# Kernel tuning notes

Measured on AMD Instinct MI355X. Metric: run time of the kernel, lower is better.

## Reference

```python
import jax, jax.numpy as jnp
import numpy as np

D, NH, E, F = 768, 12, 4, 3072            # embed dim, heads, experts/group, expert ffn (4*D)
NBLK, DEPTH = 2, 6                        # MoE blocks, DiT depth
N_A, N_B, N_C = 64, 32, 192               # group token counts
MA, FH, TC = 32, 8, 7                     # max_agents, future_horizon, traj_channels
BATCH = 8
T_TRAJ = MA * FH                          # 256 trajectory tokens
TFREQ = 256                               # sinusoidal timestep embedding dim
HD = D // NH

def _ln(x):
    mu = jnp.mean(x, -1, keepdims=True)
    v = jnp.var(x, -1, keepdims=True)
    return (x - mu) * jax.lax.rsqrt(v + 1e-6)

def _heads(x):
    b, n, _ = x.shape
    return x.reshape(b, n, NH, HD).transpose(0, 2, 1, 3)

def _attn(q, k, v):
    s = jnp.einsum('bhqd,bhkd->bhqk', q, k) * (HD ** -0.5)
    p = jax.nn.softmax(s, -1)
    o = jnp.einsum('bhqk,bhkd->bhqd', p, v)
    b, h, n, d = o.shape
    return o.transpose(0, 2, 1, 3).reshape(b, n, h * d)

def _cross(q_in, kv_in, W):
    # W: [4, D, D] = (Wq, Wk, Wv, Wo)
    q = _heads(q_in @ W[0]); k = _heads(kv_in @ W[1]); v = _heads(kv_in @ W[2])
    return _attn(q, k, v) @ W[3]

def _moe(x, Wr, W1, W2):
    # top-1 switch routing: gate = softmax prob of selected expert
    gates = jax.nn.softmax(x @ Wr)                       # [B,N,E]
    idx = jnp.argmax(gates, -1)                          # [B,N]
    gval = jnp.take_along_axis(gates, idx[..., None], -1)  # [B,N,1]
    h = jax.nn.gelu(jnp.einsum('bnd,edf->bnef', x, W1))
    y = jnp.einsum('bnef,efd->bned', h, W2)
    sel = jax.nn.one_hot(idx, W1.shape[0], dtype=x.dtype) * gval
    return jnp.einsum('bned,bne->bnd', y, sel)

def _forward(x_traj, tokens_A, tokens_B, tokens_C, W_traj, b_traj, W_ftime,
             Wt1, bt1, Wt2, bt2, moe_attn_W, moe_router, moe_W1, moe_W2,
             dit_qkv, dit_qkv_b, dit_proj, dit_proj_b, dit_mlp1, dit_mlp1_b,
             dit_mlp2, dit_mlp2_b, dit_ada, dit_ada_b,
             out_ada_W, out_ada_b, out_W, out_b, t):
    B = x_traj.shape[0]
    # timestep conditioning (DiT TimestepEmbedder)
    half = TFREQ // 2
    freqs = jnp.exp(-np.log(10000.0) * jnp.arange(half, dtype=jnp.float32) / half)
    ang = t.astype(jnp.float32)[:, None] * freqs
    temb = jnp.concatenate([jnp.cos(ang), jnp.sin(ang)], -1)     # [B,TFREQ]
    c = jax.nn.silu(temb @ Wt1 + bt1) @ Wt2 + bt2                # [B,D]

    # trajectory embedding + future-time embedding
    traj = x_traj.reshape(B, T_TRAJ, TC) @ W_traj + b_traj       # [B,256,D]
    traj = traj + jnp.tile(W_ftime, (MA, 1))[None]

    # StackedMoEBlocks: directed cross-attn A->C->B + per-group top-1 expert routing
    a, bg, cg = tokens_A, tokens_B, tokens_C
    for i in range(NBLK):
        cg = cg + _cross(_ln(cg), a, moe_attn_W[i, 0])
        bg = bg + _cross(_ln(bg), cg, moe_attn_W[i, 1])
        a = a + _moe(_ln(a), moe_router[i, 0], moe_W1[i, 0], moe_W2[i, 0])
        bg = bg + _moe(_ln(bg), moe_router[i, 1], moe_W1[i, 1], moe_W2[i, 1])
        cg = cg + _moe(_ln(cg), moe_router[i, 2], moe_W1[i, 2], moe_W2[i, 2])

    # DiT backbone over [traj | A | B | C], adaLN-zero conditioning on c
    x = jnp.concatenate([traj, a, bg, cg], 1)                    # [B,544,D]
    for i in range(DEPTH):
        mod = (jax.nn.silu(c) @ dit_ada[i] + dit_ada_b[i]).reshape(B, 6, 1, D)
        s1, sc1, g1, s2, sc2, g2 = [mod[:, j] for j in range(6)]
        h = _ln(x) * (1 + sc1) + s1
        qkv = h @ dit_qkv[i] + dit_qkv_b[i]
        q, k, v = jnp.split(qkv, 3, -1)
        x = x + g1 * (_attn(_heads(q), _heads(k), _heads(v)) @ dit_proj[i] + dit_proj_b[i])
        h = _ln(x) * (1 + sc2) + s2
        x = x + g2 * (jax.nn.gelu(h @ dit_mlp1[i] + dit_mlp1_b[i]) @ dit_mlp2[i] + dit_mlp2_b[i])

    # output head: final adaLN + projection to noise(+sigma), trajectory tokens only
    shift, scale = jnp.split(jax.nn.silu(c) @ out_ada_W + out_ada_b, 2, -1)
    h = _ln(x) * (1 + scale[:, None]) + shift[:, None]
    out = h @ out_W + out_b
    return out[:, :T_TRAJ].reshape(B, MA, FH, 2 * TC)

def setup_inputs() -> dict:
    key = jax.random.key(0)
    ks = jax.random.split(key, 24)
    n = jax.random.normal
    s = 0.02
    return dict(
        x_traj=n(ks[0], (BATCH, MA, FH, TC), jnp.float32),
        t=jax.random.randint(ks[1], (BATCH,), 0, 50),
        tokens_A=n(ks[2], (BATCH, N_A, D), jnp.float32),
        tokens_B=n(ks[3], (BATCH, N_B, D), jnp.float32),
        tokens_C=n(ks[4], (BATCH, N_C, D), jnp.float32),
        W_traj=n(ks[5], (TC, D)) * s, b_traj=jnp.zeros((D,)),
        W_ftime=n(ks[6], (FH, D)) * s,
        Wt1=n(ks[7], (TFREQ, D)) * s, bt1=jnp.zeros((D,)),
        Wt2=n(ks[8], (D, D)) * s, bt2=jnp.zeros((D,)),
        moe_attn_W=n(ks[9], (NBLK, 2, 4, D, D)) * s,
        moe_router=n(ks[10], (NBLK, 3, D, E)) * s,
        moe_W1=n(ks[11], (NBLK, 3, E, D, F)) * s,
        moe_W2=n(ks[12], (NBLK, 3, E, F, D)) * s,
        dit_qkv=n(ks[13], (DEPTH, D, 3 * D)) * s, dit_qkv_b=jnp.zeros((DEPTH, 3 * D)),
        dit_proj=n(ks[14], (DEPTH, D, D)) * s, dit_proj_b=jnp.zeros((DEPTH, D)),
        dit_mlp1=n(ks[15], (DEPTH, D, 4 * D)) * s, dit_mlp1_b=jnp.zeros((DEPTH, 4 * D)),
        dit_mlp2=n(ks[16], (DEPTH, 4 * D, D)) * s, dit_mlp2_b=jnp.zeros((DEPTH, D)),
        dit_ada=n(ks[17], (DEPTH, D, 6 * D)) * s, dit_ada_b=jnp.zeros((DEPTH, 6 * D)),
        out_ada_W=n(ks[18], (D, 2 * D)) * s, out_ada_b=jnp.zeros((2 * D,)),
        out_W=n(ks[19], (D, 2 * TC)) * s, out_b=jnp.zeros((2 * TC,)),
    )

def reference(x_traj, t, tokens_A, tokens_B, tokens_C, W_traj, b_traj, W_ftime,
              Wt1, bt1, Wt2, bt2, moe_attn_W, moe_router, moe_W1, moe_W2,
              dit_qkv, dit_qkv_b, dit_proj, dit_proj_b, dit_mlp1, dit_mlp1_b,
              dit_mlp2, dit_mlp2_b, dit_ada, dit_ada_b,
              out_ada_W, out_ada_b, out_W, out_b):
    return _forward(x_traj, tokens_A, tokens_B, tokens_C, W_traj, b_traj, W_ftime,
                    Wt1, bt1, Wt2, bt2, moe_attn_W, moe_router, moe_W1, moe_W2,
                    dit_qkv, dit_qkv_b, dit_proj, dit_proj_b, dit_mlp1, dit_mlp1_b,
                    dit_mlp2, dit_mlp2_b, dit_ada, dit_ada_b,
                    out_ada_W, out_ada_b, out_W, out_b, t)
```

## Files before the change

### kernel.cpp

```cpp
#include <hip/hip_runtime.h>
#include <hip/hip_bf16.h>
#include <math.h>

#define D 768
#define NH 12
#define HD 64
#define NEXP 4
#define FF 3072
#define NBLK 2
#define DEPTH 6
#define NA 64
#define NB 32
#define NC 192
#define BATCH 8
#define TTRAJ 256
#define NTOK 544
#define MAXTOK 1536
#define MOER 2304

typedef __attribute__((ext_vector_type(8))) short short8v;
typedef __attribute__((ext_vector_type(4))) float f32x4;

__device__ __forceinline__ float siluf(float v) { return v / (1.f + expf(-v)); }
__device__ __forceinline__ float geluf(float v) {
// ... 76 lines not shown
        __syncthreads();
        #pragma unroll
        for (int kk = 0; kk < 16; ++kk) {
            float a[4], bv[4];
            #pragma unroll
            for (int i = 0; i < 4; ++i) a[i] = As[kk][ty * 4 + i];
            #pragma unroll
            for (int j = 0; j < 4; ++j) bv[j] = Bs[kk][tx * 4 + j];
            #pragma unroll
            for (int i = 0; i < 4; ++i)
                #pragma unroll
                for (int j = 0; j < 4; ++j) acc[i][j] += a[i] * bv[j];
        }
        __syncthreads();
    }
    #pragma unroll
    for (int i = 0; i < 4; ++i) {
        int gr = row0 + ty * 4 + i; if (gr >= M) continue;
        #pragma unroll
        for (int j = 0; j < 4; ++j) {
            int gc = col0 + tx * 4 + j; if (gc >= N) continue;
            float v = acc[i][j] + (bias ? bias[gc] : 0.f);
            if (ACT == 1) v = siluf(v);
            if (ACT == 2) v = geluf(v);
            C[(size_t)gr * ldc + gc] = v;
        }
    }
}

__global__ __launch_bounds__(256) void transpose_cvt(
    const float* __restrict__ in, unsigned short* __restrict__ out, int K, int N)
{
    __shared__ unsigned short Ls[64][72];
    const float* src = in + (size_t)blockIdx.z * K * N;
    unsigned short* dst = out + (size_t)blockIdx.z * K * N;
    int k0 = blockIdx.y * 64, n0 = blockIdx.x * 64;
    int tid = threadIdx.x;
    int r = tid >> 2, c0 = (tid & 3) * 16;
    {
        const float* sp = src + (size_t)(k0 + r) * N + n0 + c0;
        #pragma unroll
        for (int j = 0; j < 16; j += 4) {
            float4 f = *(const float4*)(sp + j);
            Ls[c0 + j + 0][r] = f2bf(f.x);
            Ls[c0 + j + 1][r] = f2bf(f.y);
            Ls[c0 + j + 2][r] = f2bf(f.z);
            Ls[c0 + j + 3][r] = f2bf(f.w);
        }
    }
    __syncthreads();
    {
        unsigned short tmp[16];
        #pragma unroll
        for (int j = 0; j < 16; ++j) tmp[j] = Ls[r][c0 + j];
        unsigned short* dp = dst + (size_t)(n0 + r) * K + k0 + c0;
        *(short8v*)dp = *(short8v*)tmp;
        *(short8v*)(dp + 8) = *(short8v*)(tmp + 8);
    }
}

template<int ACT, int OUT, int TN>
__global__ __launch_bounds__(256) void gemm_lds(
    const unsigned short* __restrict__ A,
    const unsigned short* __restrict__ BT,
    const float* __restrict__ bias,
    float* __restrict__ Cf, unsigned short* __restrict__ Cb, int ldc,
    int K, int qscale_cols,
    const float* __restrict__ mod, int modstride, int gchunk, int ntok, int mrows,
    size_t bt_zs = 0, size_t bias_zs = 0, size_t c_zs = 0)
{
    constexpr int NCF = TN / 32;
    constexpr int NBS = TN / 64;
    if (bt_zs) BT += (size_t)blockIdx.z * bt_zs;
    if (bias && bias_zs) bias += (size_t)blockIdx.z * bias_zs;
    if (c_zs) { if (Cf) Cf += (size_t)blockIdx.z * c_zs; if (Cb) Cb += (size_t)blockIdx.z * c_zs; }
    __shared__ unsigned short As[2][128 * 32];
    __shared__ unsigned short Bs[2][TN * 32];
    int tid = threadIdx.x, w = tid >> 6, lane = tid & 63;
    int row0 = blockIdx.y * 128, col0 = blockIdx.x * TN;
    int wrow = (w >> 1) * 64, wcol = (w & 1) * (TN / 2);
    int lr = lane & 15, g = lane >> 4;
    f32x4 acc[4][NCF] = {};

    int ra[2], ka[2], la[2];
    #pragma unroll
    for (int i = 0; i < 2; ++i) {
        int off = tid * 16 + i * 4096;
        int row = off >> 6;
        int slot = (off >> 4) & 3;
        ra[i] = row;
        ka[i] = (slot ^ ((row >> 1) & 3)) * 8;
        la[i] = off >> 1;
    }
    int nt = K >> 5, cur = 0;
    #pragma unroll
    for (int i = 0; i < 2; ++i)
        gl16(A + (size_t)(row0 + ra[i]) * K + ka[i], &As[0][la[i]]);
    #pragma unroll
    for (int i = 0; i < NBS; ++i)
        gl16(BT + (size_t)(col0 + ra[i]) * K + ka[i], &Bs[0][la[i]]);

    for (int t = 0; t < nt; ++t) {
        __syncthreads();
        if (t + 1 < nt) {
            int k0 = (t + 1) << 5;
            #pragma unroll
            for (int i = 0; i < 2; ++i)
                gl16(A + (size_t)(row0 + ra[i]) * K + k0 + ka[i], &As[cur ^ 1][la[i]]);
            #pragma unroll
            for (int i = 0; i < NBS; ++i)
                gl16(BT + (size_t)(col0 + ra[i]) * K + k0 + ka[i], &Bs[cur ^ 1][la[i]]);
        }
        short8v av[4], bv[NCF];
        #pragma unroll
        for (int mr = 0; mr < 4; ++mr) {
            int row = wrow + mr * 16 + lr;
            av[mr] = *(const short8v*)&As[cur][row * 32 + (g ^ ((row >> 1) & 3)) * 8];
        }
        #pragma unroll
        for (int nc = 0; nc < NCF; ++nc) {
            int row = wcol + nc * 16 + lr;
            bv[nc] = *(const short8v*)&Bs[cur][row * 32 + (g ^ ((row >> 1) & 3)) * 8];
        }
        #pragma unroll
        for (int mr = 0; mr < 4; ++mr)
            #pragma unroll
            for (int nc = 0; nc < NCF; ++nc)
                acc[mr][nc] = __builtin_amdgcn_mfma_f32_16x16x32_bf16(
                    av[mr], bv[nc], acc[mr][nc], 0, 0, 0);
        cur ^= 1;
    }
    int rbase = g * 4;
    #pragma unroll
    for (int mr = 0; mr < 4; ++mr) {
        #pragma unroll
        for (int nc = 0; nc < NCF; ++nc) {
            int gc = col0 + wcol + nc * 16 + lr;
            float bb = bias ? bias[gc] : 0.f;
            #pragma unroll
            for (int r = 0; r < 4; ++r) {
                int gr = row0 + wrow + mr * 16 + rbase + r;
                if (gr >= mrows) continue;
                float v = acc[mr][nc][r] + bb;
                if (ACT == 1) v = siluf(v);
                if (ACT == 2) v = geluf(v);
                if (OUT == 0) {
                    Cf[(size_t)gr * ldc + gc] = v;
                } else if (OUT == 1) {
                    if (gc < qscale_cols) v *= 0.125f;
                    Cb[(size_t)gr * ldc + gc] = f2bf(v);
                } else {
                    float gg = 1.f;
                    if (mod) gg = mod[(size_t)(gr / ntok) * modstride + gchunk * D + gc];
                    Cf[(size_t)gr * ldc + gc] += gg * v;
                }
            }
        }
    }
}

template<int ACT>
__global__ __launch_bounds__(512, 4) void gemm_lds256(
    const unsigned short* __restrict__ A,
    const unsigned short* __restrict__ BT,
    const float* __restrict__ bias,
    unsigned short* __restrict__ Cb, int ldc,
    int K, int qscale_cols)
{
    __shared__ unsigned short As[2][256 * 32];
    __shared__ unsigned short Bs[2][128 * 32];
    int tid = threadIdx.x, w = tid >> 6, lane = tid & 63;
    int row0 = blockIdx.y * 256, col0 = blockIdx.x * 128;
    int wrow = (w >> 1) * 64, wcol = (w & 1) * 64;
    int lr = lane & 15, g = lane >> 4;
    f32x4 acc[4][4] = {};

    int ra[2], ka[2], la[2];
    #pragma unroll
    for (int i = 0; i < 2; ++i) {
        int off = tid * 16 + i * 8192;
        int row = off >> 6;
        int slot = (off >> 4) & 3;
        ra[i] = row;
        ka[i] = (slot ^ ((row >> 1) & 3)) * 8;
        la[i] = off >> 1;
    }
    int rb, kb, lb;
    {
        int off = tid * 16;
        int row = off >> 6;
        int slot = (off >> 4) & 3;
        rb = row;
        kb = (slot ^ ((row >> 1) & 3)) * 8;
        lb = off >> 1;
    }
    int nt = K >> 5, cur = 0;
    #pragma unroll
    for (int i = 0; i < 2; ++i)
        gl16(A + (size_t)(row0 + ra[i]) * K + ka[i], &As[0][la[i]]);
    gl16(BT + (size_t)(col0 + rb) * K + kb, &Bs[0][lb]);

    for (int t = 0; t < nt; ++t) {
        __syncthreads();
        if (t + 1 < nt) {
            int k0 = (t + 1) << 5;
            #pragma unroll
            for (int i = 0; i < 2; ++i)
                gl16(A + (size_t)(row0 + ra[i]) * K + k0 + ka[i], &As[cur ^ 1][la[i]]);
            gl16(BT + (size_t)(col0 + rb) * K + k0 + kb, &Bs[cur ^ 1][lb]);
        }
        short8v av[4], bv[4];
        #pragma unroll
        for (int mr = 0; mr < 4; ++mr) {
            int row = wrow + mr * 16 + lr;
            av[mr] = *(const short8v*)&As[cur][row * 32 + (g ^ ((row >> 1) & 3)) * 8];
        }
        #pragma unroll
        for (int nc = 0; nc < 4; ++nc) {
            int row = wcol + nc * 16 + lr;
            bv[nc] = *(const short8v*)&Bs[cur][row * 32 + (g ^ ((row >> 1) & 3)) * 8];
        }
        #pragma unroll
        for (int mr = 0; mr < 4; ++mr)
            #pragma unroll
            for (int nc = 0; nc < 4; ++nc)
                acc[mr][nc] = __builtin_amdgcn_mfma_f32_16x16x32_bf16(
                    av[mr], bv[nc], acc[mr][nc], 0, 0, 0);
        cur ^= 1;
    }
    int rbase = g * 4;
    int wrow2 = (w >> 1) * 64;
    (void)wrow2;
    #pragma unroll
    for (int mr = 0; mr < 4; ++mr) {
        #pragma unroll
        for (int nc = 0; nc < 4; ++nc) {
            int gc = col0 + wcol + nc * 16 + lr;
            float bb = bias ? bias[gc] : 0.f;
            #pragma unroll
            for (int r = 0; r < 4; ++r) {
                int gr = row0 + wrow + mr * 16 + rbase + r;
                float v = acc[mr][nc][r] + bb;
                if (ACT == 2) v = geluf(v);
                if (gc < qscale_cols) v *= 0.125f;
                Cb[(size_t)gr * ldc + gc] = f2bf(v);
            }
        }
    }
}

template<int PHASE>
__global__ __launch_bounds__(256) void moe_lds(
    const unsigned short* __restrict__ A,
    const unsigned short* __restrict__ BTconv,
    float* __restrict__ Cf, unsigned short* __restrict__ Cb,
    const int* __restrict__ cnt, const int* __restrict__ list,
    const float* __restrict__ gval, int RT, int egbase)
{
    constexpr int K  = (PHASE == 1) ? 768 : 3072;
    constexpr int TN = (PHASE == 1) ? 128 : 64;
    constexpr int NCF = TN / 32;
    constexpr int NBS = TN / 64;
    int egl = blockIdx.y / RT, rt = blockIdx.y % RT;
    int eg = egbase + egl;
    int c0 = cnt[eg];
    int mbase = rt * 128;
    if (mbase >= c0) return;
    int mcount = min(128, c0 - mbase);
    __shared__ int toks[128];
    int tid = threadIdx.x, w = tid >> 6, lane = tid & 63;
    if (tid < 128) toks[tid] = list[eg * MAXTOK + mbase + min(tid, mcount - 1)];
    __syncthreads();

    __shared__ unsigned short As[2][128 * 32];
    __shared__ unsigned short Bs[2][TN * 32];
    const unsigned short* BT = BTconv + (size_t)egl * (768 * 3072);
    int col0 = blockIdx.x * TN;
    int wrow = (w >> 1) * 64, wcol = (w & 1) * (TN / 2);
    int lr = lane & 15, g = lane >> 4;
    f32x4 acc[4][NCF] = {};

    int ra[2], ka[2], la[2], tok_s[2];
    #pragma unroll
    for (int i = 0; i < 2; ++i) {
        int off = tid * 16 + i * 4096;
        int row = off >> 6;
        int slot = (off >> 4) & 3;
        ra[i] = row;
        ka[i] = (slot ^ ((row >> 1) & 3)) * 8;
        la[i] = off >> 1;
        tok_s[i] = toks[row];
    }
    int nt = K >> 5, cur = 0;
    #pragma unroll
    for (int i = 0; i < 2; ++i)
        gl16(A + (size_t)tok_s[i] * K + ka[i], &As[0][la[i]]);
    #pragma unroll
    for (int i = 0; i < NBS; ++i)
        gl16(BT + (size_t)(col0 + ra[i]) * K + ka[i], &Bs[0][la[i]]);

    for (int t = 0; t < nt; ++t) {
        __syncthreads();
        if (t + 1 < nt) {
            int k0 = (t + 1) << 5;
            #pragma unroll
            for (int i = 0; i < 2; ++i)
                gl16(A + (size_t)tok_s[i] * K + k0 + ka[i], &As[cur ^ 1][la[i]]);
            #pragma unroll
            for (int i = 0; i < NBS; ++i)
                gl16(BT + (size_t)(col0 + ra[i]) * K + k0 + ka[i], &Bs[cur ^ 1][la[i]]);
        }
        short8v av[4], bv[NCF];
        #pragma unroll
        for (int mr = 0; mr < 4; ++mr) {
            int row = wrow + mr * 16 + lr;
            av[mr] = *(const short8v*)&As[cur][row * 32 + (g ^ ((row >> 1) & 3)) * 8];
        }
        #pragma unroll
        for (int nc = 0; nc < NCF; ++nc) {
            int row = wcol + nc * 16 + lr;
            bv[nc] = *(const short8v*)&Bs[cur][row * 32 + (g ^ ((row >> 1) & 3)) * 8];
        }
        #pragma unroll
        for (int mr = 0; mr < 4; ++mr)
            #pragma unroll
            for (int nc = 0; nc < NCF; ++nc)
                acc[mr][nc] = __builtin_amdgcn_mfma_f32_16x16x32_bf16(
                    av[mr], bv[nc], acc[mr][nc], 0, 0, 0);
        cur ^= 1;
    }
    int rbase = g * 4;
    #pragma unroll
    for (int mr = 0; mr < 4; ++mr) {
        #pragma unroll
        for (int r = 0; r < 4; ++r) {
            int m = wrow + mr * 16 + rbase + r;
            if (m >= mcount) continue;
            int tok = toks[m];
            #pragma unroll
            for (int nc = 0; nc < NCF; ++nc) {
                int gc = col0 + wcol + nc * 16 + lr;
                float v = acc[mr][nc][r];
                if (PHASE == 1) Cb[(size_t)tok * 3072 + gc] = f2bf(geluf(v));
                else            Cf[(size_t)tok * 768 + gc] += gval[tok] * v;
            }
        }
    }
}

__global__ __launch_bounds__(256) void ln_kernel(
    const float* __restrict__ X, unsigned short* __restrict__ Y, int R, int ntok,
    const float* __restrict__ mod, int modstride, int shift_chunk, int scale_chunk)
{
    int r = blockIdx.x;
    if (r >= R) return;
    const float* xr = X + (size_t)r * D;
    int tid = threadIdx.x;
    int lane = tid & 63, wid = tid >> 6;
    float v0 = xr[tid], v1 = xr[tid + 256], v2 = xr[tid + 512];
    float s = v0 + v1 + v2;
    float s2 = v0 * v0 + v1 * v1 + v2 * v2;
    for (int off = 32; off > 0; off >>= 1) {
        s += __shfl_xor(s, off, 64);
        s2 += __shfl_xor(s2, off, 64);
    }
    __shared__ float shs[4], shs2[4];
    if (lane == 0) { shs[wid] = s; shs2[wid] = s2; }
    __syncthreads();
    float tot = shs[0] + shs[1] + shs[2] + shs[3];
    float tot2 = shs2[0] + shs2[1] + shs2[2] + shs2[3];
    float mu = tot * (1.f / 768.f);
    float var = tot2 * (1.f / 768.f) - mu * mu;
    float rs = rsqrtf(var + 1e-6f);
    int bb = r / ntok;
    float vv[3] = {v0, v1, v2};
    #pragma unroll
    for (int j = 0; j < 3; ++j) {
        int col = tid + j * 256;
        float nrm = (vv[j] - mu) * rs;
        float y = nrm;
        if (mod) {
            float scv = mod[(size_t)bb * modstride + scale_chunk * D + col];
            float shv = mod[(size_t)bb * modstride + shift_chunk * D + col];
            y = nrm * (1.f + scv) + shv;
        }
        Y[(size_t)r * D + col] = f2bf(y);
    }
}

__global__ __launch_bounds__(512) void attn_mfma(
    const unsigned short* __restrict__ Qp, int ldq, int qoff,
    const unsigned short* __restrict__ Kp, int ldk, int koff,
    const unsigned short* __restrict__ Vp, int ldv, int voff,
    unsigned short* __restrict__ O, int ldo,
    int Nq, int Nkv)
{
    __shared__ unsigned short Qs[128 * 64];
    __shared__ unsigned short Ks[64 * 64];
    __shared__ unsigned short Vs[64 * 64];
    __shared__ unsigned short Ps[128 * 64];
    int h = blockIdx.y, b = blockIdx.z, q0 = blockIdx.x * 128;
    int tid = threadIdx.x, w = tid >> 6, lane = tid & 63;
    int wrow = w * 16;
    int lr = lane & 15, g = lane >> 4;

    {
        int srow = tid >> 2, sc = (tid & 3) * 16;
        int gr = min(q0 + srow, Nq - 1);
        const unsigned short* qp = Qp + (size_t)(b * Nq + gr) * ldq + qoff + h * 64 + sc;
        short8v v0 = *(const short8v*)qp, v1 = *(const short8v*)(qp + 8);
        int s0 = sc >> 3;
        *(short8v*)&Qs[srow * 64 + (s0 ^ (srow & 7)) * 8] = v0;
        *(short8v*)&Qs[srow * 64 + ((s0 + 1) ^ (srow & 7)) * 8] = v1;
    }
    float m_r[4] = {-1e30f, -1e30f, -1e30f, -1e30f};
    float l_r[4] = {};
    f32x4 acc0 = {}, acc1 = {}, acc2 = {}, acc3 = {};

    for (int kv0 = 0; kv0 < Nkv; kv0 += 64) {
        {
            int t2 = tid & 255;
            int srow = t2 >> 2, sc = (t2 & 3) * 16;
            int gc = min(kv0 + srow, Nkv - 1);
            if (tid < 256) {
                const unsigned short* kp = Kp + (size_t)(b * Nkv + gc) * ldk + koff + h * 64 + sc;
                short8v v0 = *(const short8v*)kp, v1 = *(const short8v*)(kp + 8);
                int s0 = sc >> 3;
                *(short8v*)&Ks[srow * 64 + (s0 ^ (srow & 7)) * 8] = v0;
                *(short8v*)&Ks[srow * 64 + ((s0 + 1) ^ (srow & 7)) * 8] = v1;
            } else {
                const unsigned short* vp = Vp + (size_t)(b * Nkv + gc) * ldv + voff + h * 64 + sc;
                #pragma unroll
                for (int j = 0; j < 16; ++j) {
                    int d = sc + j;
                    Vs[d * 64 + (((srow >> 3) ^ (d & 7)) * 8) + (srow & 7)] = vp[j];
                }
            }
        }
        __syncthreads();
        short8v aq0, aq1;
        {
            int row = wrow + lr;
            aq0 = *(const short8v*)&Qs[row * 64 + ((0 + g) ^ (row & 7)) * 8];
            aq1 = *(const short8v*)&Qs[row * 64 + ((4 + g) ^ (row & 7)) * 8];
        }
        f32x4 sf[4];
        #pragma unroll
        for (int nc = 0; nc < 4; ++nc) {
            int row = nc * 16 + lr;
            short8v bk0 = *(const short8v*)&Ks[row * 64 + ((0 + g) ^ (row & 7)) * 8];
            short8v bk1 = *(const short8v*)&Ks[row * 64 + ((4 + g) ^ (row & 7)) * 8];
            f32x4 z = {};
            z = __builtin_amdgcn_mfma_f32_16x16x32_bf16(aq0, bk0, z, 0, 0, 0);
            sf[nc] = __builtin_amdgcn_mfma_f32_16x16x32_bf16(aq1, bk1, z, 0, 0, 0);
        }
        bool val0 = (kv0 + 0 * 16 + lr) < Nkv;
        bool val1 = (kv0 + 1 * 16 + lr) < Nkv;
        bool val2 = (kv0 + 2 * 16 + lr) < Nkv;
        bool val3 = (kv0 + 3 * 16 + lr) < Nkv;
        float fs[4];
        #pragma unroll
        for (int r = 0; r < 4; ++r) {
            float s0 = val0 ? sf[0][r] : -1e30f;
            float s1 = val1 ? sf[1][r] : -1e30f;
            float s2 = val2 ? sf[2][r] : -1e30f;
            float s3 = val3 ? sf[3][r] : -1e30f;
            float mx = fmaxf(fmaxf(s0, s1), fmaxf(s2, s3));
            mx = fmaxf(mx, __shfl_xor(mx, 1, 64));
            mx = fmaxf(mx, __shfl_xor(mx, 2, 64));
            mx = fmaxf(mx, __shfl_xor(mx, 4, 64));
            mx = fmaxf(mx, __shfl_xor(mx, 8, 64));
            float mn = fmaxf(m_r[r], mx);
            fs[r] = __expf(m_r[r] - mn);
            m_r[r] = mn;
            float p0 = __expf(s0 - mn), p1 = __expf(s1 - mn);
            float p2 = __expf(s2 - mn), p3 = __expf(s3 - mn);
            float rsum = p0 + p1 + p2 + p3;
            rsum += __shfl_xor(rsum, 1, 64);
            rsum += __shfl_xor(rsum, 2, 64);
            rsum += __shfl_xor(rsum, 4, 64);
            rsum += __shfl_xor(rsum, 8, 64);
            l_r[r] = l_r[r] * fs[r] + rsum;
            int ql = wrow + g * 4 + r;
            int base = ql * 64;
            int x7 = ql & 7;
            Ps[base + (((0 * 16 + lr) >> 3) ^ x7) * 8 + (lr & 7)] = f2bf(p0);
            Ps[base + (((1 * 16 + lr) >> 3) ^ x7) * 8 + (lr & 7)] = f2bf(p1);
            Ps[base + (((2 * 16 + lr) >> 3) ^ x7) * 8 + (lr & 7)] = f2bf(p2);
            Ps[base + (((3 * 16 + lr) >> 3) ^ x7) * 8 + (lr & 7)] = f2bf(p3);
            acc0[r] *= fs[r]; acc1[r] *= fs[r]; acc2[r] *= fs[r]; acc3[r] *= fs[r];
        }
        __syncthreads();
        short8v ap0, ap1;
        {
            int row = wrow + lr;
            ap0 = *(const short8v*)&Ps[row * 64 + ((0 + g) ^ (row & 7)) * 8];
            ap1 = *(const short8v*)&Ps[row * 64 + ((4 + g) ^ (row & 7)) * 8];
        }
        {
            int row = 0 * 16 + lr;
            short8v b0 = *(const short8v*)&Vs[row * 64 + ((0 + g) ^ (row & 7)) * 8];
            short8v b1 = *(const short8v*)&Vs[row * 64 + ((4 + g) ^ (row & 7)) * 8];
            acc0 = __builtin_amdgcn_mfma_f32_16x16x32_bf16(ap0, b0, acc0, 0, 0, 0);
            acc0 = __builtin_amdgcn_mfma_f32_16x16x32_bf16(ap1, b1, acc0, 0, 0, 0);
        }
        {
            int row = 1 * 16 + lr;
            short8v b0 = *(const short8v*)&Vs[row * 64 + ((0 + g) ^ (row & 7)) * 8];
            short8v b1 = *(const short8v*)&Vs[row * 64 + ((4 + g) ^ (row & 7)) * 8];
            acc1 = __builtin_amdgcn_mfma_f32_16x16x32_bf16(ap0, b0, acc1, 0, 0, 0);
            acc1 = __builtin_amdgcn_mfma_f32_16x16x32_bf16(ap1, b1, acc1, 0, 0, 0);
        }
        {
            int row = 2 * 16 + lr;
            short8v b0 = *(const short8v*)&Vs[row * 64 + ((0 + g) ^ (row & 7)) * 8];
            short8v b1 = *(const short8v*)&Vs[row * 64 + ((4 + g) ^ (row & 7)) * 8];
            acc2 = __builtin_amdgcn_mfma_f32_16x16x32_bf16(ap0, b0, acc2, 0, 0, 0);
            acc2 = __builtin_amdgcn_mfma_f32_16x16x32_bf16(ap1, b1, acc2, 0, 0, 0);
        }
        {
            int row = 3 * 16 + lr;
            short8v b0 = *(const short8v*)&Vs[row * 64 + ((0 + g) ^ (row & 7)) * 8];
            short8v b1 = *(const short8v*)&Vs[row * 64 + ((4 + g) ^ (row & 7)) * 8];
            acc3 = __builtin_amdgcn_mfma_f32_16x16x32_bf16(ap0, b0, acc3, 0, 0, 0);
            acc3 = __builtin_amdgcn_mfma_f32_16x16x32_bf16(ap1, b1, acc3, 0, 0, 0);
        }
        __syncthreads();
    }
    #pragma unroll
    for (int r = 0; r < 4; ++r) {
        int ql = wrow + g * 4 + r;
        if (q0 + ql >= Nq) continue;
        float rl = 1.f / l_r[r];
        unsigned short* op = O + (size_t)(b * Nq + q0 + ql) * ldo + h * 64 + lr;
        op[0]  = f2bf(acc0[r] * rl);
        op[16] = f2bf(acc1[r] * rl);
        op[32] = f2bf(acc2[r] * rl);
        op[48] = f2bf(acc3[r] * rl);
    }
}

__global__ __launch_bounds__(64) void router_kernel(
    const unsigned short* __restrict__ X, const float* __restrict__ WrBase,
    int* __restrict__ idx, float* __restrict__ gval)
{
    int tkn = blockIdx.x; int lane = threadIdx.x;
    int grp = (tkn >= 768) ? 2 : (tkn >= 512 ? 1 : 0);
    const float* Wr = WrBase + (size_t)grp * D * NEXP;
    const unsigned short* xr = X + (size_t)tkn * D;
    float p0 = 0, p1 = 0, p2 = 0, p3 = 0;
    for (int dd = lane; dd < D; dd += 64) {
        float xv = bf2f(xr[dd]);
        const float* wq = Wr + dd * 4;
        p0 += xv * wq[0]; p1 += xv * wq[1]; p2 += xv * wq[2]; p3 += xv * wq[3];
    }
    for (int off = 32; off > 0; off >>= 1) {
        p0 += __shfl_xor(p0, off, 64); p1 += __shfl_xor(p1, off, 64);
        p2 += __shfl_xor(p2, off, 64); p3 += __shfl_xor(p3, off, 64);
    }
    if (lane == 0) {
        float best = p0; int e = 0;
        if (p1 > best) { best = p1; e = 1; }
        if (p2 > best) { best = p2; e = 2; }
        if (p3 > best) { best = p3; e = 3; }
        float sum = expf(p0 - best) + expf(p1 - best) + expf(p2 - best) + expf(p3 - best);
        idx[tkn] = grp * 4 + e;
        gval[tkn] = 1.f / sum;
    }
}

__global__ __launch_bounds__(256) void scatter_kernel(
    const int* __restrict__ idx, int* __restrict__ cnt,
    int* __restrict__ list, int ntok)
{
    __shared__ int lcnt[12];
    int tid = threadIdx.x;
    if (tid < 12) lcnt[tid] = 0;
    __syncthreads();
    for (int i = tid; i < ntok; i += 256) {
        int e = idx[i];
        int pos = atomicAdd(&lcnt[e], 1);
        list[e * MAXTOK + pos] = i;
    }
    __syncthreads();
    if (tid < 12) cnt[tid] = lcnt[tid];
}

__global__ void concat_kernel(const float* __restrict__ traj, const float* __restrict__ a,
                              const float* __restrict__ bg, const float* __restrict__ cg,
                              float* __restrict__ x, int total)
{
    int i = blockIdx.x * blockDim.x + threadIdx.x;
    if (i >= total) return;
    int col = i % D;
    int r = i / D;
    int n = r % NTOK, b = r / NTOK;
    float v;
    if (n < 256)      v = traj[((size_t)b * 256 + n) * D + col];
    else if (n < 320) v = a[((size_t)b * 64 + (n - 256)) * D + col];
    else if (n < 352) v = bg[((size_t)b * 32 + (n - 320)) * D + col];
    else              v = cg[((size_t)b * 192 + (n - 352)) * D + col];
    x[i] = v;
}

__global__ void head_prep(const float* __restrict__ W, unsigned short* __restrict__ WT14) {
    int i = blockIdx.x * blockDim.x + threadIdx.x;
    if (i >= 14 * 768) return;
    int o = i / 768, d = i % 768;
    WT14[i] = f2bf(W[d * 14 + o]);
}

__global__ __launch_bounds__(64) void head_kernel(
    const unsigned short* __restrict__ lnb, const unsigned short* __restrict__ WT14,
    const float* __restrict__ bias, float* __restrict__ out)
{
    int r = blockIdx.x;
    int b = r >> 8, n = r & 255;
    const unsigned short* hrow = lnb + (size_t)(b * NTOK + n) * D;
    int l = threadIdx.x;
    if (l >= 56) return;
    int o = l >> 2, p = l & 3;
    const unsigned short* hp = hrow + p * 192;
    const unsigned short* wp = WT14 + o * 768 + p * 192;
    float acc = 0.f;
    for (int i = 0; i < 192; i += 8) {
        short8v hv = *(const short8v*)(hp + i);
        short8v wv = *(const short8v*)(wp + i);
        #pragma unroll
        for (int j = 0; j < 8; ++j)
            acc += bf2f((unsigned short)hv[j]) * bf2f((unsigned short)wv[j]);
    }
    acc += __shfl_xor(acc, 1, 64);
    acc += __shfl_xor(acc, 2, 64);
    if (p == 0) out[(size_t)r * 14 + o] = acc + bias[o];
}

static inline void tcvt(const float* W, unsigned short* WT, int K, int N, int z, hipStream_t s) {
    transpose_cvt<<<dim3(N / 64, K / 64, z), 256, 0, s>>>(W, WT, K, N);
}
static inline void g_bf(int act, const unsigned short* A, const unsigned short* BT,
                        const float* bias, unsigned short* C, int ldc,
                        int M, int N, int K, int qcols, hipStream_t s)
{
    if (M % 256 == 0 && N % 128 == 0 && N >= 2304) {
        dim3 g(N / 128, M / 256);
        if (act == 2) gemm_lds256<2><<<g, 512, 0, s>>>(A, BT, bias, C, ldc, K, qcols);
        else          gemm_lds256<0><<<g, 512, 0, s>>>(A, BT, bias, C, ldc, K, qcols);
        return;
    }
    if (N != 768) {
        dim3 g(N / 128, M / 128);
        if (act == 2) gemm_lds<2, 1, 128><<<g, 256, 0, s>>>(A, BT, bias, nullptr, C, ldc, K, qcols, nullptr, 0, 0, 1, 1 << 30);
        else          gemm_lds<0, 1, 128><<<g, 256, 0, s>>>(A, BT, bias, nullptr, C, ldc, K, qcols, nullptr, 0, 0, 1, 1 << 30);
    } else {
        dim3 g(N / 64, M / 128);
        if (act == 2) gemm_lds<2, 1, 64><<<g, 256, 0, s>>>(A, BT, bias, nullptr, C, ldc, K, qcols, nullptr, 0, 0, 1, 1 << 30);
        else          gemm_lds<0, 1, 64><<<g, 256, 0, s>>>(A, BT, bias, nullptr, C, ldc, K, qcols, nullptr, 0, 0, 1, 1 << 30);
    }
}
static inline void g_res(const unsigned short* A, const unsigned short* BT,
                         const float* bias, float* C, int ldc, int M, int N, int K,
                         const float* mod, int modstride, int gchunk, int ntok, hipStream_t s)
{
    dim3 g(N / 64, M / 128);
    gemm_lds<0, 2, 64><<<g, 256, 0, s>>>(A, BT, bias, C, nullptr, ldc, K, 0, mod, modstride, gchunk, ntok, 1 << 30);
}

extern "C" void kernel_launch(void* const* d_in, const int* in_sizes, int n_in,
                              void* d_out, int out_size, void* d_ws, size_t ws_size,
                              hipStream_t stream)
{
    const float* x_traj   = (const float*)d_in[0];
    const int*   t_arr    = (const int*)d_in[1];
    const float* tokA     = (const float*)d_in[2];
    const float* tokB     = (const float*)d_in[3];
    const float* tokC     = (const float*)d_in[4];
    const float* W_traj   = (const float*)d_in[5];
    const float* b_traj   = (const float*)d_in[6];
    const float* W_ftime  = (const float*)d_in[7];
    const float* Wt1      = (const float*)d_in[8];
    const float* bt1      = (const float*)d_in[9];
    const float* Wt2      = (const float*)d_in[10];
    const float* bt2      = (const float*)d_in[11];
    const float* moe_attn = (const float*)d_in[12];
    const float* moe_rout = (const float*)d_in[13];
    const float* moe_W1   = (const float*)d_in[14];
    const float* moe_W2   = (const float*)d_in[15];
    const float* dit_qkv  = (const float*)d_in[16];
    const float* dit_qkvb = (const float*)d_in[17];
    const float* dit_proj = (const float*)d_in[18];
    const float* dit_projb= (const float*)d_in[19];
    const float* dit_mlp1 = (const float*)d_in[20];
    const float* dit_mlp1b= (const float*)d_in[21];
    const float* dit_mlp2 = (const float*)d_in[22];
    const float* dit_mlp2b= (const float*)d_in[23];
    const float* dit_ada  = (const float*)d_in[24];
    const float* dit_adab = (const float*)d_in[25];
    const float* out_adaW = (const float*)d_in[26];
    const float* out_adab = (const float*)d_in[27];
    const float* out_W    = (const float*)d_in[28];
    const float* out_b    = (const float*)d_in[29];
    float* out = (float*)d_out;
    float* ws = (float*)d_ws;

    const size_t o_cnt  = 14336;
    const size_t o_idx  = 14400;
    const size_t o_gval = 16704;
    const size_t o_list = 19008;
    const size_t o_traj = 66624;
    const size_t o_a    = 1639488;
    const size_t o_bg   = 2032704;
    const size_t o_cg   = 2229312;
    const size_t o_x    = 3408960;
    const size_t o_lnb  = 6751296;
    const size_t o_qkvb = 8422464;
    const size_t o_attnO= 13435968;
    const size_t o_h    = 15107136;
    const size_t o_kvbf = 23561280;
    const size_t o_wt   = 24151104;
    const size_t o_wt14 = 28869696;
    const size_t o_tembP= 28875072;
    const size_t o_ub   = 28891456;
    const size_t o_scb  = 28940608;
    const size_t o_mod  = o_traj;
    const size_t o_mod2 = o_traj + 221184;

    const size_t o_wqkv  = 29000000;
    const size_t o_wproj = 34308416;
    const size_t o_wmlp1 = 36077888;
    const size_t o_wmlp2 = 43155776;
    const size_t o_wada  = 50233664;
    const size_t o_wada2 = 60850496;
    const size_t o_wcross= 61440320;
    const size_t o_wmoe1 = 66158912;
    const size_t o_wmoe2 = 94470464;
    const bool bigw = ws_size >= (size_t)123000000 * 4;

    int* cnt_p  = (int*)(ws + o_cnt);
    int* idx_p  = (int*)(ws + o_idx);
    int* list_p = (int*)(ws + o_list);
    float* gval_p = ws + o_gval;
    unsigned short* lnb  = (unsigned short*)(ws + o_lnb);
    unsigned short* qkvb = (unsigned short*)(ws + o_qkvb);
    unsigned short* attO = (unsigned short*)(ws + o_attnO);
    unsigned short* hbuf = (unsigned short*)(ws + o_h);
    unsigned short* kvbf = (unsigned short*)(ws + o_kvbf);
    unsigned short* wt   = (unsigned short*)(ws + o_wt);
    unsigned short* wt14 = (unsigned short*)(ws + o_wt14);
    unsigned short* tembP= (unsigned short*)(ws + o_tembP);
    unsigned short* ub   = (unsigned short*)(ws + o_ub);
    unsigned short* scb  = (unsigned short*)(ws + o_scb);
    unsigned short* wqkvS = (unsigned short*)(ws + o_wqkv);
    unsigned short* wprojS= (unsigned short*)(ws + o_wproj);
    unsigned short* wmlp1S= (unsigned short*)(ws + o_wmlp1);
    unsigned short* wmlp2S= (unsigned short*)(ws + o_wmlp2);
    unsigned short* wadaS = (unsigned short*)(ws + o_wada);
    unsigned short* wada2S= (unsigned short*)(ws + o_wada2);
    unsigned short* wcrossS=(unsigned short*)(ws + o_wcross);
    unsigned short* wmoe1S= (unsigned short*)(ws + o_wmoe1);
    unsigned short* wmoe2S= (unsigned short*)(ws + o_wmoe2);
    unsigned short* c_q  = qkvb;
    unsigned short* c_kv = qkvb + 1179648;

    const size_t WSZ = (size_t)D * D;

    gemm_act<0><<<dim3(12, 32), 256, 0, stream>>>(x_traj, 7, W_traj, D, b_traj,
                                                  ws + o_traj, D, BATCH * TTRAJ, D, 7);
    add_ftime<<<(BATCH * TTRAJ * D + 255) / 256, 256, 0, stream>>>(ws + o_traj, W_ftime, BATCH * TTRAJ * D);

    hipError_t e1 = hipMemcpyAsync(ws + o_a, tokA, (size_t)BATCH * NA * D * 4, hipMemcpyDeviceToDevice, stream); (void)e1;
    hipError_t e2 = hipMemcpyAsync(ws + o_bg, tokB, (size_t)BATCH * NB * D * 4, hipMemcpyDeviceToDevice, stream); (void)e2;
    hipError_t e3 = hipMemcpyAsync(ws + o_cg, tokC, (size_t)BATCH * NC * D * 4, hipMemcpyDeviceToDevice, stream); (void)e3;
    head_prep<<<42, 256, 0, stream>>>(out_W, wt14);

    if (bigw) {
        tcvt(dit_qkv,  wqkvS,  D, 3 * D, DEPTH, stream);
        tcvt(dit_proj, wprojS, D, D, DEPTH, stream);
        tcvt(dit_mlp1, wmlp1S, D, FF, DEPTH, stream);
        tcvt(dit_mlp2, wmlp2S, FF, D, DEPTH, stream);
        tcvt(dit_ada,  wadaS,  D, 6 * D, DEPTH, stream);
        tcvt(out_adaW, wada2S, D, 2 * D, 1, stream);
        tcvt(moe_attn, wcrossS, D, D, NBLK * 2 * 4, stream);
        tcvt(moe_W1,   wmoe1S, D, FF, NBLK * 3 * NEXP, stream);
        tcvt(moe_W2,   wmoe2S, FF, D, NBLK * 3 * NEXP, stream);
    }

    timestep_kernel<<<128, 256, 0, stream>>>(t_arr, tembP);
    tcvt(Wt1, wt, 256, D, 1, stream);
    gemm_lds<1, 1, 64><<<dim3(12, 1), 256, 0, stream>>>(
        tembP, wt, bt1, nullptr, ub, D, 256, 0, nullptr, 0, 0, 1, 128);
    tcvt(Wt2, wt, D, D, 1, stream);
    gemm_lds<1, 1, 64><<<dim3(12, 1), 256, 0, stream>>>(
        ub, wt, bt2, nullptr, scb, D, D, 0, nullptr, 0, 0, 1, 128);

    for (int i = 0; i < NBLK; ++i) {
        {
            const unsigned short* Wc;
            if (bigw) Wc = wcrossS + (size_t)(i * 2 + 0) * 4 * WSZ;
            else { tcvt(moe_attn + (size_t)(i * 2 + 0) * 4 * WSZ, wt, D, D, 4, stream); Wc = wt; }
            ln_kernel<<<BATCH * NC, 256, 0, stream>>>(ws + o_cg, lnb, BATCH * NC, 1, nullptr, 0, 0, 0);
            g_bf(0, lnb, Wc, nullptr, c_q, D, BATCH * NC, D, D, 768, stream);
            cvt_bf16<<<(BATCH * NA * D / 8 + 255) / 256, 256, 0, stream>>>(ws + o_a, kvbf, BATCH * NA * D / 8);
            g_bf(0, kvbf, Wc + 1 * WSZ, nullptr, c_kv, 2 * D, BATCH * NA, 2 * D, D, 0, stream);
            attn_mfma<<<dim3((NC + 127) / 128, NH, BATCH), 512, 0, stream>>>(
                c_q, D, 0, c_kv, 2 * D, 0, c_kv, 2 * D, D, attO, D, NC, NA);
            g_res(attO, Wc + 3 * WSZ, nullptr, ws + o_cg, D, BATCH * NC, D, D, nullptr, 0, 0, 1, stream);
        }
        {
            const unsigned short* Wc;
            if (bigw) Wc = wcrossS + (size_t)(i * 2 + 1) * 4 * WSZ;
            else { tcvt(moe_attn + (size_t)(i * 2 + 1) * 4 * WSZ, wt, D, D, 4, stream); Wc = wt; }
            ln_kernel<<<BATCH * NB, 256, 0, stream>>>(ws + o_bg, lnb, BATCH * NB, 1, nullptr, 0, 0, 0);
            g_bf(0, lnb, Wc, nullptr, c_q, D, BATCH * NB, D, D, 768, stream);
            cvt_bf16<<<(BATCH * NC * D / 8 + 255) / 256, 256, 0, stream>>>(ws + o_cg, kvbf, BATCH * NC * D / 8);
            g_bf(0, kvbf, Wc + 1 * WSZ, nullptr, c_kv, 2 * D, BATCH * NC, 2 * D, D, 0, stream);
            attn_mfma<<<dim3(1, NH, BATCH), 512, 0, stream>>>(
                c_q, D, 0, c_kv, 2 * D, 0, c_kv, 2 * D, D, attO, D, NB, NC);
            g_res(attO, Wc + 3 * WSZ, nullptr, ws + o_bg, D, BATCH * NB, D, D, nullptr, 0, 0, 1, stream);
        }
        ln_kernel<<<MOER, 256, 0, stream>>>(ws + o_a, lnb, MOER, 1, nullptr, 0, 0, 0);
        router_kernel<<<MOER, 64, 0, stream>>>(lnb, moe_rout + (size_t)(i * 3) * D * NEXP, idx_p, gval_p);
        scatter_kernel<<<1, 256, 0, stream>>>(idx_p, cnt_p, list_p, MOER);
        const int RT = 12;
        if (bigw) {
            moe_lds<1><<<dim3(24, 12 * RT), 256, 0, stream>>>(
                lnb, wmoe1S + (size_t)(i * 3) * NEXP * D * FF, nullptr, hbuf,
                cnt_p, list_p, gval_p, RT, 0);
            moe_lds<2><<<dim3(12, 12 * RT), 256, 0, stream>>>(
                hbuf, wmoe2S + (size_t)(i * 3) * NEXP * D * FF, ws + o_a, nullptr,
                cnt_p, list_p, gval_p, RT, 0);
        } else {
            for (int g = 0; g < 3; ++g) {
                tcvt(moe_W1 + (size_t)(i * 3 + g) * NEXP * D * FF, wt, D, FF, NEXP, stream);
                moe_lds<1><<<dim3(24, 4 * RT), 256, 0, stream>>>(
                    lnb, wt, nullptr, hbuf, cnt_p, list_p, gval_p, RT, g * 4);
                tcvt(moe_W2 + (size_t)(i * 3 + g) * NEXP * FF * D, wt, FF, D, NEXP, stream);
                moe_lds<2><<<dim3(12, 4 * RT), 256, 0, stream>>>(
                    hbuf, wt, ws + o_a, nullptr, cnt_p, list_p, gval_p, RT, g * 4);
            }
        }
    }

    concat_kernel<<<(BATCH * NTOK * D + 255) / 256, 256, 0, stream>>>(
        ws + o_traj, ws + o_a, ws + o_bg, ws + o_cg, ws + o_x, BATCH * NTOK * D);

    if (bigw) {
        gemm_lds<0, 0, 128><<<dim3(36, 1, DEPTH), 256, 0, stream>>>(
            scb, wadaS, dit_adab, ws + o_mod, nullptr, 6 * D, D, 0,
            nullptr, 0, 0, 1, 8,
            (size_t)D * 6 * D, (size_t)6 * D, (size_t)8 * 6 * D);
        gemm_lds<0, 0, 128><<<dim3(12, 1), 256, 0, stream>>>(
            scb, wada2S, out_adab, ws + o_mod2, nullptr, 2 * D, D, 0, nullptr, 0, 0, 1, 8);
    } else {
        for (int i = 0; i < DEPTH; ++i) {
            tcvt(dit_ada + (size_t)i * D * 6 * D, wt, D, 6 * D, 1, stream);
            gemm_lds<0, 0, 128><<<dim3(36, 1), 256, 0, stream>>>(
                scb, wt, dit_adab + (size_t)i * 6 * D, ws + o_mod + (size_t)i * 8 * 6 * D,
                nullptr, 6 * D, D, 0, nullptr, 0, 0, 1, 8);
        }
        tcvt(out_adaW, wt, D, 2 * D, 1, stream);
        gemm_lds<0, 0, 128><<<dim3(12, 1), 256, 0, stream>>>(
            scb, wt, out_adab, ws + o_mod2, nullptr, 2 * D, D, 0, nullptr, 0, 0, 1, 8);
    }

    const int R = BATCH * NTOK;
    for (int i = 0; i < DEPTH; ++i) {
        const float* mod_l = ws + o_mod + (size_t)i * 8 * 6 * D;
        const unsigned short *Wq = nullptr, *Wp = nullptr, *Wm1 = nullptr, *Wm2 = nullptr;
        if (bigw) {
            Wq  = wqkvS  + (size_t)i * D * 3 * D;
            Wp  = wprojS + (size_t)i * D * D;
            Wm1 = wmlp1S + (size_t)i * D * FF;
            Wm2 = wmlp2S + (size_t)i * D * FF;
        }
        ln_kernel<<<R, 256, 0, stream>>>(ws + o_x, lnb, R, NTOK, mod_l, 6 * D, 0, 1);
        if (!bigw) { tcvt(dit_qkv + (size_t)i * D * 3 * D, wt, D, 3 * D, 1, stream); Wq = wt; }
        g_bf(0, lnb, Wq, dit_qkvb + (size_t)i * 3 * D, qkvb, 3 * D, R, 3 * D, D, 768, stream);
        attn_mfma<<<dim3((NTOK + 127) / 128, NH, BATCH), 512, 0, stream>>>(
            qkvb, 3 * D, 0, qkvb, 3 * D, D, qkvb, 3 * D, 2 * D, attO, D, NTOK, NTOK);
        if (!bigw) { tcvt(dit_proj + (size_t)i * D * D, wt, D, D, 1, stream); Wp = wt; }
        g_res(attO, Wp, dit_projb + (size_t)i * D, ws + o_x, D, R, D, D,
              mod_l, 6 * D, 2, NTOK, stream);
        ln_kernel<<<R, 256, 0, stream>>>(ws + o_x, lnb, R, NTOK, mod_l, 6 * D, 3, 4);
        if (!bigw) { tcvt(dit_mlp1 + (size_t)i * D * FF, wt, D, FF, 1, stream); Wm1 = wt; }
        g_bf(2, lnb, Wm1, dit_mlp1b + (size_t)i * FF, hbuf, FF, R, FF, D, 0, stream);
        if (!bigw) { tcvt(dit_mlp2 + (size_t)i * FF * D, wt, FF, D, 1, stream); Wm2 = wt; }
        g_res(hbuf, Wm2, dit_mlp2b + (size_t)i * D, ws + o_x, D, R, D, FF,
              mod_l, 6 * D, 5, NTOK, stream);
    }

    ln_kernel<<<R, 256, 0, stream>>>(ws + o_x, lnb, R, NTOK, ws + o_mod2, 2 * D, 0, 1);
    head_kernel<<<BATCH * TTRAJ, 64, 0, stream>>>(lnb, wt14, out_b, out);
}
```

Before: 2.379 ms.

## Store residual streams in bf16 instead of fp32 throughout the pipeline

Switches the residual buffers for the token groups and the DiT hidden state from fp32 to bf16. Residual GEMM epilogues now read-modify-write bf16, LayerNorm reads bf16, and the input token copies become direct bf16 conversions, which drops the separate cvt_bf16 passes before the K/V projections. This halves residual memory traffic and removes some kernels, but residual accumulation in bf16 loses precision across 6 DiT layers and the MoE blocks, which may hurt accuracy.

```diff
diff --git a/kernel.cpp b/kernel.cpp
--- a/kernel.cpp
+++ b/kernel.cpp
@@ -252,7 +252,8 @@
                 } else {
                     float gg = 1.f;
                     if (mod) gg = mod[(size_t)(gr / ntok) * modstride + gchunk * D + gc];
-                    Cf[(size_t)gr * ldc + gc] += gg * v;
+                    size_t idx = (size_t)gr * ldc + gc;
+                    Cb[idx] = f2bf(bf2f(Cb[idx]) + gg * v);
                 }
             }
         }
@@ -329,8 +330,6 @@
         cur ^= 1;
     }
     int rbase = g * 4;
-    int wrow2 = (w >> 1) * 64;
-    (void)wrow2;
     #pragma unroll
     for (int mr = 0; mr < 4; ++mr) {
         #pragma unroll
@@ -353,7 +352,7 @@
 __global__ __launch_bounds__(256) void moe_lds(
     const unsigned short* __restrict__ A,
     const unsigned short* __restrict__ BTconv,
-    float* __restrict__ Cf, unsigned short* __restrict__ Cb,
+    unsigned short* __restrict__ Cb,
     const int* __restrict__ cnt, const int* __restrict__ list,
     const float* __restrict__ gval, int RT, int egbase)
 {
@@ -442,22 +441,25 @@
                 int gc = col0 + wcol + nc * 16 + lr;
                 float v = acc[mr][nc][r];
                 if (PHASE == 1) Cb[(size_t)tok * 3072 + gc] = f2bf(geluf(v));
-                else            Cf[(size_t)tok * 768 + gc] += gval[tok] * v;
+                else {
+                    size_t idx = (size_t)tok * 768 + gc;
+                    Cb[idx] = f2bf(bf2f(Cb[idx]) + gval[tok] * v);
+                }
             }
         }
     }
 }
 
 __global__ __launch_bounds__(256) void ln_kernel(
-    const float* __restrict__ X, unsigned short* __restrict__ Y, int R, int ntok,
+    const unsigned short* __restrict__ X, unsigned short* __restrict__ Y, int R, int ntok,
     const float* __restrict__ mod, int modstride, int shift_chunk, int scale_chunk)
 {
     int r = blockIdx.x;
     if (r >= R) return;
-    const float* xr = X + (size_t)r * D;
+    const unsigned short* xr = X + (size_t)r * D;
     int tid = threadIdx.x;
     int lane = tid & 63, wid = tid >> 6;
-    float v0 = xr[tid], v1 = xr[tid + 256], v2 = xr[tid + 512];
+    float v0 = bf2f(xr[tid]), v1 = bf2f(xr[tid + 256]), v2 = bf2f(xr[tid + 512]);
     float s = v0 + v1 + v2;
     float s2 = v0 * v0 + v1 * v1 + v2 * v2;
     for (int off = 32; off > 0; off >>= 1) {
@@ -686,17 +688,17 @@
     if (tid < 12) cnt[tid] = lcnt[tid];
 }
 
-__global__ void concat_kernel(const float* __restrict__ traj, const float* __restrict__ a,
-                              const float* __restrict__ bg, const float* __restrict__ cg,
-                              float* __restrict__ x, int total)
+__global__ void concat_kernel(const float* __restrict__ traj, const unsigned short* __restrict__ a,
+                              const unsigned short* __restrict__ bg, const unsigned short* __restrict__ cg,
+                              unsigned short* __restrict__ x, int total)
 {
     int i = blockIdx.x * blockDim.x + threadIdx.x;
     if (i >= total) return;
     int col = i % D;
     int r = i / D;
     int n = r % NTOK, b = r / NTOK;
-    float v;
-    if (n < 256)      v = traj[((size_t)b * 256 + n) * D + col];
+    unsigned short v;
+    if (n < 256)      v = f2bf(traj[((size_t)b * 256 + n) * D + col]);
     else if (n < 320) v = a[((size_t)b * 64 + (n - 256)) * D + col];
     else if (n < 352) v = bg[((size_t)b * 32 + (n - 320)) * D + col];
     else              v = cg[((size_t)b * 192 + (n - 352)) * D + col];
@@ -759,11 +761,11 @@
     }
 }
 static inline void g_res(const unsigned short* A, const unsigned short* BT,
-                         const float* bias, float* C, int ldc, int M, int N, int K,
+                         const float* bias, unsigned short* C, int ldc, int M, int N, int K,
                          const float* mod, int modstride, int gchunk, int ntok, hipStream_t s)
 {
     dim3 g(N / 64, M / 128);
-    gemm_lds<0, 2, 64><<<g, 256, 0, s>>>(A, BT, bias, C, nullptr, ldc, K, 0, mod, modstride, gchunk, ntok, 1 << 30);
+    gemm_lds<0, 2, 64><<<g, 256, 0, s>>>(A, BT, bias, nullptr, C, ldc, K, 0, mod, modstride, gchunk, ntok, 1 << 30);
 }
 
 extern "C" void kernel_launch(void* const* d_in, const int* in_sizes, int n_in,
@@ -809,14 +811,11 @@
     const size_t o_list = 19008;
     const size_t o_traj = 66624;
     const size_t o_a    = 1639488;
-    const size_t o_bg   = 2032704;
-    const size_t o_cg   = 2229312;
     const size_t o_x    = 3408960;
     const size_t o_lnb  = 6751296;
     const size_t o_qkvb = 8422464;
     const size_t o_attnO= 13435968;
     const size_t o_h    = 15107136;
-    const size_t o_kvbf = 23561280;
     const size_t o_wt   = 24151104;
     const size_t o_wt14 = 28869696;
     const size_t o_tembP= 28875072;
@@ -840,11 +839,14 @@
     int* idx_p  = (int*)(ws + o_idx);
     int* list_p = (int*)(ws + o_list);
     float* gval_p = ws + o_gval;
+    unsigned short* abf  = (unsigned short*)(ws + o_a);
+    unsigned short* bgbf = abf + 512 * 768;
+    unsigned short* cgbf = abf + 768 * 768;
+    unsigned short* xbf  = (unsigned short*)(ws + o_x);
     unsigned short* lnb  = (unsigned short*)(ws + o_lnb);
     unsigned short* qkvb = (unsigned short*)(ws + o_qkvb);
     unsigned short* attO = (unsigned short*)(ws + o_attnO);
     unsigned short* hbuf = (unsigned short*)(ws + o_h);
-    unsigned short* kvbf = (unsigned short*)(ws + o_kvbf);
     unsigned short* wt   = (unsigned short*)(ws + o_wt);
     unsigned short* wt14 = (unsigned short*)(ws + o_wt14);
     unsigned short* tembP= (unsigned short*)(ws + o_tembP);
@@ -868,9 +870,9 @@
                                                   ws + o_traj, D, BATCH * TTRAJ, D, 7);
     add_ftime<<<(BATCH * TTRAJ * D + 255) / 256, 256, 0, stream>>>(ws + o_traj, W_ftime, BATCH * TTRAJ * D);
 
-    hipError_t e1 = hipMemcpyAsync(ws + o_a, tokA, (size_t)BATCH * NA * D * 4, hipMemcpyDeviceToDevice, stream); (void)e1;
-    hipError_t e2 = hipMemcpyAsync(ws + o_bg, tokB, (size_t)BATCH * NB * D * 4, hipMemcpyDeviceToDevice, stream); (void)e2;
-    hipError_t e3 = hipMemcpyAsync(ws + o_cg, tokC, (size_t)BATCH * NC * D * 4, hipMemcpyDeviceToDevice, stream); (void)e3;
+    cvt_bf16<<<(512 * 768 / 8 + 255) / 256, 256, 0, stream>>>(tokA, abf, 512 * 768 / 8);
+    cvt_bf16<<<(256 * 768 / 8 + 255) / 256, 256, 0, stream>>>(tokB, bgbf, 256 * 768 / 8);
+    cvt_bf16<<<(1536 * 768 / 8 + 255) / 256, 256, 0, stream>>>(tokC, cgbf, 1536 * 768 / 8);
     head_prep<<<42, 256, 0, stream>>>(out_W, wt14);
 
     if (bigw) {
@@ -898,51 +900,49 @@
             const unsigned short* Wc;
             if (bigw) Wc = wcrossS + (size_t)(i * 2 + 0) * 4 * WSZ;
             else { tcvt(moe_attn + (size_t)(i * 2 + 0) * 4 * WSZ, wt, D, D, 4, stream); Wc = wt; }
-            ln_kernel<<<BATCH * NC, 256, 0, stream>>>(ws + o_cg, lnb, BATCH * NC, 1, nullptr, 0, 0, 0);
+            ln_kernel<<<BATCH * NC, 256, 0, stream>>>(cgbf, lnb, BATCH * NC, 1, nullptr, 0, 0, 0);
             g_bf(0, lnb, Wc, nullptr, c_q, D, BATCH * NC, D, D, 768, stream);
-            cvt_bf16<<<(BATCH * NA * D / 8 + 255) / 256, 256, 0, stream>>>(ws + o_a, kvbf, BATCH * NA * D / 8);
-            g_bf(0, kvbf, Wc + 1 * WSZ, nullptr, c_kv, 2 * D, BATCH * NA, 2 * D, D, 0, stream);
+            g_bf(0, abf, Wc + 1 * WSZ, nullptr, c_kv, 2 * D, BATCH * NA, 2 * D, D, 0, stream);
             attn_mfma<<<dim3((NC + 127) / 128, NH, BATCH), 512, 0, stream>>>(
                 c_q, D, 0, c_kv, 2 * D, 0, c_kv, 2 * D, D, attO, D, NC, NA);
-            g_res(attO, Wc + 3 * WSZ, nullptr, ws + o_cg, D, BATCH * NC, D, D, nullptr, 0, 0, 1, stream);
+            g_res(attO, Wc + 3 * WSZ, nullptr, cgbf, D, BATCH * NC, D, D, nullptr, 0, 0, 1, stream);
         }
         {
             const unsigned short* Wc;
             if (bigw) Wc = wcrossS + (size_t)(i * 2 + 1) * 4 * WSZ;
             else { tcvt(moe_attn + (size_t)(i * 2 + 1) * 4 * WSZ, wt, D, D, 4, stream); Wc = wt; }
-            ln_kernel<<<BATCH * NB, 256, 0, stream>>>(ws + o_bg, lnb, BATCH * NB, 1, nullptr, 0, 0, 0);
+            ln_kernel<<<BATCH * NB, 256, 0, stream>>>(bgbf, lnb, BATCH * NB, 1, nullptr, 0, 0, 0);
             g_bf(0, lnb, Wc, nullptr, c_q, D, BATCH * NB, D, D, 768, stream);
-            cvt_bf16<<<(BATCH * NC * D / 8 + 255) / 256, 256, 0, stream>>>(ws + o_cg, kvbf, BATCH * NC * D / 8);
-            g_bf(0, kvbf, Wc + 1 * WSZ, nullptr, c_kv, 2 * D, BATCH * NC, 2 * D, D, 0, stream);
+            g_bf(0, cgbf, Wc + 1 * WSZ, nullptr, c_kv, 2 * D, BATCH * NC, 2 * D, D, 0, stream);
             attn_mfma<<<dim3(1, NH, BATCH), 512, 0, stream>>>(
                 c_q, D, 0, c_kv, 2 * D, 0, c_kv, 2 * D, D, attO, D, NB, NC);
-            g_res(attO, Wc + 3 * WSZ, nullptr, ws + o_bg, D, BATCH * NB, D, D, nullptr, 0, 0, 1, stream);
-        }
-        ln_kernel<<<MOER, 256, 0, stream>>>(ws + o_a, lnb, MOER, 1, nullptr, 0, 0, 0);
+            g_res(attO, Wc + 3 * WSZ, nullptr, bgbf, D, BATCH * NB, D, D, nullptr, 0, 0, 1, stream);
+        }
+        ln_kernel<<<MOER, 256, 0, stream>>>(abf, lnb, MOER, 1, nullptr, 0, 0, 0);
         router_kernel<<<MOER, 64, 0, stream>>>(lnb, moe_rout + (size_t)(i * 3) * D * NEXP, idx_p, gval_p);
         scatter_kernel<<<1, 256, 0, stream>>>(idx_p, cnt_p, list_p, MOER);
         const int RT = 12;
         if (bigw) {
             moe_lds<1><<<dim3(24, 12 * RT), 256, 0, stream>>>(
-                lnb, wmoe1S + (size_t)(i * 3) * NEXP * D * FF, nullptr, hbuf,
+                lnb, wmoe1S + (size_t)(i * 3) * NEXP * D * FF, hbuf,
                 cnt_p, list_p, gval_p, RT, 0);
             moe_lds<2><<<dim3(12, 12 * RT), 256, 0, stream>>>(
-                hbuf, wmoe2S + (size_t)(i * 3) * NEXP * D * FF, ws + o_a, nullptr,
+                hbuf, wmoe2S + (size_t)(i * 3) * NEXP * D * FF, abf,
                 cnt_p, list_p, gval_p, RT, 0);
         } else {
             for (int g = 0; g < 3; ++g) {
                 tcvt(moe_W1 + (size_t)(i * 3 + g) * NEXP * D * FF, wt, D, FF, NEXP, stream);
                 moe_lds<1><<<dim3(24, 4 * RT), 256, 0, stream>>>(
-                    lnb, wt, nullptr, hbuf, cnt_p, list_p, gval_p, RT, g * 4);
+                    lnb, wt, hbuf, cnt_p, list_p, gval_p, RT, g * 4);
                 tcvt(moe_W2 + (size_t)(i * 3 + g) * NEXP * FF * D, wt, FF, D, NEXP, stream);
                 moe_lds<2><<<dim3(12, 4 * RT), 256, 0, stream>>>(
-                    hbuf, wt, ws + o_a, nullptr, cnt_p, list_p, gval_p, RT, g * 4);
+                    hbuf, wt, abf, cnt_p, list_p, gval_p, RT, g * 4);
             }
         }
     }
 
     concat_kernel<<<(BATCH * NTOK * D + 255) / 256, 256, 0, stream>>>(
-        ws + o_traj, ws + o_a, ws + o_bg, ws + o_cg, ws + o_x, BATCH * NTOK * D);
+        ws + o_traj, abf, bgbf, cgbf, xbf, BATCH * NTOK * D);
 
     if (bigw) {
         gemm_lds<0, 0, 128><<<dim3(36, 1, DEPTH), 256, 0, stream>>>(
@@ -973,22 +973,22 @@
             Wm1 = wmlp1S + (size_t)i * D * FF;
             Wm2 = wmlp2S + (size_t)i * D * FF;
         }
-        ln_kernel<<<R, 256, 0, stream>>>(ws + o_x, lnb, R, NTOK, mod_l, 6 * D, 0, 1);
+        ln_kernel<<<R, 256, 0, stream>>>(xbf, lnb, R, NTOK, mod_l, 6 * D, 0, 1);
         if (!bigw) { tcvt(dit_qkv + (size_t)i * D * 3 * D, wt, D, 3 * D, 1, stream); Wq = wt; }
         g_bf(0, lnb, Wq, dit_qkvb + (size_t)i * 3 * D, qkvb, 3 * D, R, 3 * D, D, 768, stream);
         attn_mfma<<<dim3((NTOK + 127) / 128, NH, BATCH), 512, 0, stream>>>(
             qkvb, 3 * D, 0, qkvb, 3 * D, D, qkvb, 3 * D, 2 * D, attO, D, NTOK, NTOK);
         if (!bigw) { tcvt(dit_proj + (size_t)i * D * D, wt, D, D, 1, stream); Wp = wt; }
-        g_res(attO, Wp, dit_projb + (size_t)i * D, ws + o_x, D, R, D, D,
+        g_res(attO, Wp, dit_projb + (size_t)i * D, xbf, D, R, D, D,
               mod_l, 6 * D, 2, NTOK, stream);
-        ln_kernel<<<R, 256, 0, stream>>>(ws + o_x, lnb, R, NTOK, mod_l, 6 * D, 3, 4);
+        ln_kernel<<<R, 256, 0, stream>>>(xbf, lnb, R, NTOK, mod_l, 6 * D, 3, 4);
         if (!bigw) { tcvt(dit_mlp1 + (size_t)i * D * FF, wt, D, FF, 1, stream); Wm1 = wt; }
         g_bf(2, lnb, Wm1, dit_mlp1b + (size_t)i * FF, hbuf, FF, R, FF, D, 0, stream);
         if (!bigw) { tcvt(dit_mlp2 + (size_t)i * FF * D, wt, FF, D, 1, stream); Wm2 = wt; }
-        g_res(hbuf, Wm2, dit_mlp2b + (size_t)i * D, ws + o_x, D, R, D, FF,
+        g_res(hbuf, Wm2, dit_mlp2b + (size_t)i * D, xbf, D, R, D, FF,
               mod_l, 6 * D, 5, NTOK, stream);
     }
 
-    ln_kernel<<<R, 256, 0, stream>>>(ws + o_x, lnb, R, NTOK, ws + o_mod2, 2 * D, 0, 1);
+    ln_kernel<<<R, 256, 0, stream>>>(xbf, lnb, R, NTOK, ws + o_mod2, 2 * D, 0, 1);
     head_kernel<<<BATCH * TTRAJ, 64, 0, stream>>>(lnb, wt14, out_b, out);
 }
```

New measurement: 2.356 ms. Within noise of the previous version (-1.0%).
